# Kernel optimization log

Measured on AMD Instinct MI355X. Metric: run time of the kernel, lower is better.

The kernel has to match this reference:

```python
import jax, jax.numpy as jnp
import numpy as np


def setup_inputs() -> dict:
    key = jax.random.key(0)
    kq, kk, kv, km = jax.random.split(key, 4)
    B, H, S, D = 2, 16, 2048, 64
    q = jax.random.normal(kq, (B, H, S, D), dtype=jnp.float32)
    k = jax.random.normal(kk, (B, H, S, D), dtype=jnp.float32)
    v = jax.random.normal(kv, (B, H, S, D), dtype=jnp.float32)
    mask = jax.random.randint(km, (B, 1, S, S), 0, 2, dtype=jnp.int32)
    return {"q": q, "k": k, "v": v, "mask": mask}


def reference(q, k, v, mask):
    # Scaled dot-product attention: softmax(Q K^T / sqrt(D)) V
    D = q.shape[-1]
    scale = jnp.asarray(1.0 / np.sqrt(D), q.dtype)
    score = jnp.einsum("bhqd,bhkd->bhqk", q, k) * scale  # [B,H,S,S]
    score = jnp.where(mask == 0, jnp.asarray(-10000.0, score.dtype), score)
    attn = jax.nn.softmax(score, axis=-1)
    out = jnp.einsum("bhqk,bhkd->bhqd", attn, v)  # [B,H,S,D]
    return (out, attn)
```

## Files before the change

### kernel.cpp

```cpp
#include <hip/hip_runtime.h>
#include <stdint.h>

typedef __attribute__((ext_vector_type(8))) short short8;
typedef __attribute__((ext_vector_type(4))) float f32x4;

#define B_ 2
#define H_ 16
#define S_ 2048
#define D_ 64
#define KB_ 64
#define NT_ (S_ / KB_)

union PKU { unsigned u[4]; short8 s; };

__device__ __forceinline__ unsigned pk2(float x, float y) {
  const unsigned a = __builtin_bit_cast(unsigned, x) + 0x8000u;
  const unsigned b = __builtin_bit_cast(unsigned, y) + 0x8000u;
  return (a >> 16) | (b & 0xffff0000u);
}

__global__ __launch_bounds__(256, 4)
void attn_kernel(const float* __restrict__ Q, const float* __restrict__ K,
                 const float* __restrict__ V, const int* __restrict__ M,
                 float* __restrict__ O, float* __restrict__ A)
{
  const int bid = blockIdx.x + (blockIdx.y << 5);
  const int qt  = (bid >> 3) & 31;
  const int bh  = (bid & 7) | ((bid >> 8) << 3);
  const int b   = bh >> 4;

  const int tid  = threadIdx.x;
  const int wave = tid >> 6;
  const int lane = tid & 63;
  const int l15  = lane & 15;
  const int quad = lane >> 4;

  const float* Qp = Q + (size_t)bh * S_ * D_;
  const float* Kp = K + (size_t)bh * S_ * D_;
  const float* Vp = V + (size_t)bh * S_ * D_;
  const int*   Mp = M + (size_t)b * S_ * S_;
  float* Op = O + (size_t)bh * S_ * D_;
  float* Ap = A + (size_t)bh * S_ * S_;

  const int q0 = qt * 64 + wave * 16;

  __shared__ __attribute__((aligned(16))) short Ks[64][72];
  __shared__ __attribute__((aligned(16))) short Vt[64][72];
  __shared__ __attribute__((aligned(16))) float Ps[4][16][68];
  short* Pb = (short*)&Ps[wave][0][0];

  short8 aq[2];
  {
    const float* qr = Qp + (size_t)(q0 + l15) * D_ + quad * 8;
#pragma unroll
    for (int h = 0; h < 2; ++h) {
      const float4 x0 = *(const float4*)(qr + h * 32);
      const float4 x1 = *(const float4*)(qr + h * 32 + 4);
      PKU u;
      u.u[0] = pk2(x0.x * 0.125f, x0.y * 0.125f);
      u.u[1] = pk2(x0.z * 0.125f, x0.w * 0.125f);
      u.u[2] = pk2(x1.x * 0.125f, x1.y * 0.125f);
      u.u[3] = pk2(x1.z * 0.125f, x1.w * 0.125f);
      aq[h] = u.s;
    }
  }

  const int ksr  = tid >> 2;
  const int ksc  = (tid & 3) * 4;
  const int vd   = tid & 7;
  const int vk   = (tid >> 3) * 2;
  const int lrow = lane >> 4;
  const int lcol = (lane & 15) * 4;

  float kbuf[16];
  float vbuf[16];

  auto loadK = [&](int kt) {
#pragma unroll
    for (int j = 0; j < 4; ++j) {
      const float4 x = *(const float4*)(Kp + (size_t)(kt + ksr) * D_ + ksc + 16 * j);
      kbuf[4*j+0] = x.x; kbuf[4*j+1] = x.y; kbuf[4*j+2] = x.z; kbuf[4*j+3] = x.w;
    }
  };
  auto writeK = [&]() {
#pragma unroll
    for (int j = 0; j < 4; ++j)
      *(uint2*)&Ks[ksr][ksc + 16*j] =
        make_uint2(pk2(kbuf[4*j+0], kbuf[4*j+1]), pk2(kbuf[4*j+2], kbuf[4*j+3]));
  };
  auto loadV = [&](int kt) {
    const float* vr = Vp + (size_t)(kt + vk) * D_ + vd;
#pragma unroll
    for (int j = 0; j < 8; ++j) {
      vbuf[j]   = vr[8*j];
      vbuf[8+j] = vr[D_ + 8*j];
    }
  };
  auto writeV = [&]() {
#pragma unroll
    for (int j = 0; j < 8; ++j)
      *(unsigned*)&Vt[vd + 8*j][vk] = pk2(vbuf[j], vbuf[8+j]);
  };

  float lr[4];

  {
    float rowsum[4] = {0.f, 0.f, 0.f, 0.f};
    loadK(0);
    writeK();
    __syncthreads();
    for (int t = 0; t < NT_; ++t) {
      const int kt = t * KB_;
      if (t + 1 < NT_) loadK(kt + KB_);
      int4 mr[4];
#pragma unroll
      for (int i = 0; i < 4; ++i)
        mr[i] = *(const int4*)(Mp + (size_t)(q0 + lrow + 4*i) * S_ + kt + lcol);

      f32x4 acc[4] = {{0,0,0,0},{0,0,0,0},{0,0,0,0},{0,0,0,0}};
#pragma unroll
      for (int nt = 0; nt < 4; ++nt)
#pragma unroll
        for (int h = 0; h < 2; ++h) {
          const short8 bk = *(const short8*)&Ks[nt*16 + l15][h*32 + quad*8];
          acc[nt] = __builtin_amdgcn_mfma_f32_16x16x32_bf16(aq[h], bk, acc[nt], 0, 0, 0);
        }
#pragma unroll
      for (int nt = 0; nt < 4; ++nt)
#pragma unroll
        for (int r = 0; r < 4; ++r)
          Ps[wave][quad*4 + r][nt*16 + l15] = acc[nt][r];
      __asm__ volatile("s_waitcnt lgkmcnt(0)" ::: "memory");
#pragma unroll
      for (int i = 0; i < 4; ++i) {
        const f32x4 s = *(const f32x4*)&Ps[wave][lrow + 4*i][lcol];
        const float e0 = mr[i].x ? __expf(s[0]) : 0.f;
        const float e1 = mr[i].y ? __expf(s[1]) : 0.f;
        const float e2 = mr[i].z ? __expf(s[2]) : 0.f;
        const float e3 = mr[i].w ? __expf(s[3]) : 0.f;
        rowsum[i] += (e0 + e1) + (e2 + e3);
      }
      __syncthreads();
      if (t + 1 < NT_) writeK();
      __syncthreads();
    }
#pragma unroll
    for (int i = 0; i < 4; ++i) {
      float s = rowsum[i];
      s += __shfl_xor(s, 1);
      s += __shfl_xor(s, 2);
      s += __shfl_xor(s, 4);
      s += __shfl_xor(s, 8);
      lr[i] = (s > 0.f) ? -__logf(s) : 0.f;
    }
  }

  f32x4 oacc[4] = {{0,0,0,0},{0,0,0,0},{0,0,0,0},{0,0,0,0}};
  loadK(0);
  loadV(0);
  writeK();
  writeV();
  __syncthreads();
  for (int t = 0; t < NT_; ++t) {
    const int kt = t * KB_;
    if (t + 1 < NT_) { loadK(kt + KB_); loadV(kt + KB_); }
    int4 mr[4];
#pragma unroll
    for (int i = 0; i < 4; ++i)
      mr[i] = *(const int4*)(Mp + (size_t)(q0 + lrow + 4*i) * S_ + kt + lcol);

    f32x4 acc[4] = {{0,0,0,0},{0,0,0,0},{0,0,0,0},{0,0,0,0}};
#pragma unroll
    for (int nt = 0; nt < 4; ++nt)
#pragma unroll
      for (int h = 0; h < 2; ++h) {
        const short8 bk = *(const short8*)&Ks[nt*16 + l15][h*32 + quad*8];
        acc[nt] = __builtin_amdgcn_mfma_f32_16x16x32_bf16(aq[h], bk, acc[nt], 0, 0, 0);
      }
#pragma unroll
    for (int nt = 0; nt < 4; ++nt)
#pragma unroll
      for (int r = 0; r < 4; ++r)
        Ps[wave][quad*4 + r][nt*16 + l15] = acc[nt][r];
    __asm__ volatile("s_waitcnt lgkmcnt(0)" ::: "memory");

    f32x4 sr[4];
#pragma unroll
    for (int i = 0; i < 4; ++i)
      sr[i] = *(const f32x4*)&Ps[wave][lrow + 4*i][lcol];
    __asm__ volatile("s_waitcnt lgkmcnt(0)" ::: "memory");

#pragma unroll
    for (int i = 0; i < 4; ++i) {
      const float lv = lr[i];
      f32x4 p;
      p[0] = __expf(mr[i].x ? sr[i][0] + lv : -1e5f);
      p[1] = __expf(mr[i].y ? sr[i][1] + lv : -1e5f);
      p[2] = __expf(mr[i].z ? sr[i][2] + lv : -1e5f);
      p[3] = __expf(mr[i].w ? sr[i][3] + lv : -1e5f);
      __builtin_nontemporal_store(p, (f32x4*)(Ap + (size_t)(q0 + lrow + 4*i) * S_ + kt + lcol));
      *(uint2*)&Pb[(lrow + 4*i) * 72 + lcol] =
        make_uint2(pk2(p[0], p[1]), pk2(p[2], p[3]));
    }
    __asm__ volatile("s_waitcnt lgkmcnt(0)" ::: "memory");

    const short8 pa0 = *(const short8*)&Pb[l15 * 72 + quad * 8];
    const short8 pa1 = *(const short8*)&Pb[l15 * 72 + 32 + quad * 8];
#pragma unroll
    for (int nt = 0; nt < 4; ++nt) {
      const short8 bv0 = *(const short8*)&Vt[nt*16 + l15][quad*8];
      const short8 bv1 = *(const short8*)&Vt[nt*16 + l15][32 + quad*8];
      oacc[nt] = __builtin_amdgcn_mfma_f32_16x16x32_bf16(pa0, bv0, oacc[nt], 0, 0, 0);
      oacc[nt] = __builtin_amdgcn_mfma_f32_16x16x32_bf16(pa1, bv1, oacc[nt], 0, 0, 0);
    }
    __syncthreads();
    if (t + 1 < NT_) { writeK(); writeV(); }
    __syncthreads();
  }

#pragma unroll
  for (int nt = 0; nt < 4; ++nt)
#pragma unroll
    for (int r = 0; r < 4; ++r)
      Op[(size_t)(q0 + quad*4 + r) * D_ + nt*16 + l15] = oacc[nt][r];
}

extern "C" void kernel_launch(void* const* d_in, const int* in_sizes, int n_in,
                              void* d_out, int out_size, void* d_ws, size_t ws_size,
                              hipStream_t stream) {
  const float* q = (const float*)d_in[0];
  const float* k = (const float*)d_in[1];
  const float* v = (const float*)d_in[2];
  const int*   m = (const int*)d_in[3];
  float* out  = (float*)d_out;
  float* attn = out + (size_t)B_ * H_ * S_ * D_;

  dim3 grid(S_ / 64, B_ * H_);
  attn_kernel<<<grid, 256, 0, stream>>>(q, k, v, m, out, attn);
}
```

Baseline: 731.1 us.

## Vectorize V loads with swizzled transpose, add setprio, simplify P staging and barriers

V tiles are now loaded with coalesced float4 reads and transposed into LDS with an XOR swizzle on the key index, replacing strided scalar global loads. MFMA sections are wrapped in s_setprio to favour matrix issue. P is stored to LDS as fp32 and repacked to bf16 when read, instead of being written as bf16 into an aliased buffer. __syncthreads is replaced by a raw waitcnt+s_barrier. Scalar 16-bit LDS writes for V and the extra fp32 LDS traffic for P may add LDS cost.

```diff
diff --git a/kernel.cpp b/kernel.cpp
--- a/kernel.cpp
+++ b/kernel.cpp
@@ -11,12 +11,20 @@
 #define KB_ 64
 #define NT_ (S_ / KB_)
 
-union PKU { unsigned u[4]; short8 s; };
-
 __device__ __forceinline__ unsigned pk2(float x, float y) {
   const unsigned a = __builtin_bit_cast(unsigned, x) + 0x8000u;
   const unsigned b = __builtin_bit_cast(unsigned, y) + 0x8000u;
   return (a >> 16) | (b & 0xffff0000u);
+}
+__device__ __forceinline__ short b16(float x) {
+  return (short)((__builtin_bit_cast(unsigned, x) + 0x8000u) >> 16);
+}
+
+__device__ __forceinline__ void block_barrier() {
+  __asm__ volatile("s_waitcnt lgkmcnt(0)\n\ts_barrier" ::: "memory");
+}
+__device__ __forceinline__ void lgkm0() {
+  __asm__ volatile("s_waitcnt lgkmcnt(0)" ::: "memory");
 }
 
 __global__ __launch_bounds__(256, 4)
@@ -47,7 +55,6 @@
   __shared__ __attribute__((aligned(16))) short Ks[64][72];
   __shared__ __attribute__((aligned(16))) short Vt[64][72];
   __shared__ __attribute__((aligned(16))) float Ps[4][16][68];
-  short* Pb = (short*)&Ps[wave][0][0];
 
   short8 aq[2];
   {
@@ -56,7 +63,7 @@
     for (int h = 0; h < 2; ++h) {
       const float4 x0 = *(const float4*)(qr + h * 32);
       const float4 x1 = *(const float4*)(qr + h * 32 + 4);
-      PKU u;
+      union { unsigned u[4]; short8 s; } u;
       u.u[0] = pk2(x0.x * 0.125f, x0.y * 0.125f);
       u.u[1] = pk2(x0.z * 0.125f, x0.w * 0.125f);
       u.u[2] = pk2(x1.x * 0.125f, x1.y * 0.125f);
@@ -65,10 +72,8 @@
     }
   }
 
-  const int ksr  = tid >> 2;
-  const int ksc  = (tid & 3) * 4;
-  const int vd   = tid & 7;
-  const int vk   = (tid >> 3) * 2;
+  const int srow = tid >> 2;
+  const int scol = (tid & 3) * 4;
   const int lrow = lane >> 4;
   const int lcol = (lane & 15) * 4;
 
@@ -78,28 +83,31 @@
   auto loadK = [&](int kt) {
 #pragma unroll
     for (int j = 0; j < 4; ++j) {
-      const float4 x = *(const float4*)(Kp + (size_t)(kt + ksr) * D_ + ksc + 16 * j);
+      const float4 x = *(const float4*)(Kp + (size_t)(kt + srow) * D_ + scol + 16 * j);
       kbuf[4*j+0] = x.x; kbuf[4*j+1] = x.y; kbuf[4*j+2] = x.z; kbuf[4*j+3] = x.w;
     }
   };
   auto writeK = [&]() {
 #pragma unroll
     for (int j = 0; j < 4; ++j)
-      *(uint2*)&Ks[ksr][ksc + 16*j] =
+      *(uint2*)&Ks[srow][scol + 16*j] =
         make_uint2(pk2(kbuf[4*j+0], kbuf[4*j+1]), pk2(kbuf[4*j+2], kbuf[4*j+3]));
   };
   auto loadV = [&](int kt) {
-    const float* vr = Vp + (size_t)(kt + vk) * D_ + vd;
-#pragma unroll
-    for (int j = 0; j < 8; ++j) {
-      vbuf[j]   = vr[8*j];
-      vbuf[8+j] = vr[D_ + 8*j];
+#pragma unroll
+    for (int u = 0; u < 4; ++u) {
+      const float4 x = *(const float4*)(Vp + (size_t)(kt + srow) * D_ + scol + 16 * u);
+      vbuf[4*u+0] = x.x; vbuf[4*u+1] = x.y; vbuf[4*u+2] = x.z; vbuf[4*u+3] = x.w;
     }
   };
   auto writeV = [&]() {
 #pragma unroll
-    for (int j = 0; j < 8; ++j)
-      *(unsigned*)&Vt[vd + 8*j][vk] = pk2(vbuf[j], vbuf[8+j]);
+    for (int u = 0; u < 4; ++u) {
+      const int kks = srow ^ (u << 4);
+#pragma unroll
+      for (int c = 0; c < 4; ++c)
+        Vt[16*u + scol + c][kks] = b16(vbuf[4*u+c]);
+    }
   };
 
   float lr[4];
@@ -108,7 +116,7 @@
     float rowsum[4] = {0.f, 0.f, 0.f, 0.f};
     loadK(0);
     writeK();
-    __syncthreads();
+    block_barrier();
     for (int t = 0; t < NT_; ++t) {
       const int kt = t * KB_;
       if (t + 1 < NT_) loadK(kt + KB_);
@@ -118,6 +126,7 @@
         mr[i] = *(const int4*)(Mp + (size_t)(q0 + lrow + 4*i) * S_ + kt + lcol);
 
       f32x4 acc[4] = {{0,0,0,0},{0,0,0,0},{0,0,0,0},{0,0,0,0}};
+      __builtin_amdgcn_s_setprio(1);
 #pragma unroll
       for (int nt = 0; nt < 4; ++nt)
 #pragma unroll
@@ -125,12 +134,13 @@
           const short8 bk = *(const short8*)&Ks[nt*16 + l15][h*32 + quad*8];
           acc[nt] = __builtin_amdgcn_mfma_f32_16x16x32_bf16(aq[h], bk, acc[nt], 0, 0, 0);
         }
+      __builtin_amdgcn_s_setprio(0);
 #pragma unroll
       for (int nt = 0; nt < 4; ++nt)
 #pragma unroll
         for (int r = 0; r < 4; ++r)
           Ps[wave][quad*4 + r][nt*16 + l15] = acc[nt][r];
-      __asm__ volatile("s_waitcnt lgkmcnt(0)" ::: "memory");
+      lgkm0();
 #pragma unroll
       for (int i = 0; i < 4; ++i) {
         const f32x4 s = *(const f32x4*)&Ps[wave][lrow + 4*i][lcol];
@@ -140,9 +150,9 @@
         const float e3 = mr[i].w ? __expf(s[3]) : 0.f;
         rowsum[i] += (e0 + e1) + (e2 + e3);
       }
-      __syncthreads();
+      block_barrier();
       if (t + 1 < NT_) writeK();
-      __syncthreads();
+      block_barrier();
     }
 #pragma unroll
     for (int i = 0; i < 4; ++i) {
@@ -160,7 +170,7 @@
   loadV(0);
   writeK();
   writeV();
-  __syncthreads();
+  block_barrier();
   for (int t = 0; t < NT_; ++t) {
     const int kt = t * KB_;
     if (t + 1 < NT_) { loadK(kt + KB_); loadV(kt + KB_); }
@@ -170,6 +180,7 @@
       mr[i] = *(const int4*)(Mp + (size_t)(q0 + lrow + 4*i) * S_ + kt + lcol);
 
     f32x4 acc[4] = {{0,0,0,0},{0,0,0,0},{0,0,0,0},{0,0,0,0}};
+    __builtin_amdgcn_s_setprio(1);
 #pragma unroll
     for (int nt = 0; nt < 4; ++nt)
 #pragma unroll
@@ -177,45 +188,53 @@
         const short8 bk = *(const short8*)&Ks[nt*16 + l15][h*32 + quad*8];
         acc[nt] = __builtin_amdgcn_mfma_f32_16x16x32_bf16(aq[h], bk, acc[nt], 0, 0, 0);
       }
+    __builtin_amdgcn_s_setprio(0);
 #pragma unroll
     for (int nt = 0; nt < 4; ++nt)
 #pragma unroll
       for (int r = 0; r < 4; ++r)
         Ps[wave][quad*4 + r][nt*16 + l15] = acc[nt][r];
-    __asm__ volatile("s_waitcnt lgkmcnt(0)" ::: "memory");
-
-    f32x4 sr[4];
-#pragma unroll
-    for (int i = 0; i < 4; ++i)
-      sr[i] = *(const f32x4*)&Ps[wave][lrow + 4*i][lcol];
-    __asm__ volatile("s_waitcnt lgkmcnt(0)" ::: "memory");
+    lgkm0();
 
 #pragma unroll
     for (int i = 0; i < 4; ++i) {
+      const f32x4 s = *(const f32x4*)&Ps[wave][lrow + 4*i][lcol];
       const float lv = lr[i];
       f32x4 p;
-      p[0] = __expf(mr[i].x ? sr[i][0] + lv : -1e5f);
-      p[1] = __expf(mr[i].y ? sr[i][1] + lv : -1e5f);
-      p[2] = __expf(mr[i].z ? sr[i][2] + lv : -1e5f);
-      p[3] = __expf(mr[i].w ? sr[i][3] + lv : -1e5f);
+      p[0] = __expf(mr[i].x ? s[0] + lv : -1e5f);
+      p[1] = __expf(mr[i].y ? s[1] + lv : -1e5f);
+      p[2] = __expf(mr[i].z ? s[2] + lv : -1e5f);
+      p[3] = __expf(mr[i].w ? s[3] + lv : -1e5f);
       __builtin_nontemporal_store(p, (f32x4*)(Ap + (size_t)(q0 + lrow + 4*i) * S_ + kt + lcol));
-      *(uint2*)&Pb[(lrow + 4*i) * 72 + lcol] =
-        make_uint2(pk2(p[0], p[1]), pk2(p[2], p[3]));
-    }
-    __asm__ volatile("s_waitcnt lgkmcnt(0)" ::: "memory");
-
-    const short8 pa0 = *(const short8*)&Pb[l15 * 72 + quad * 8];
-    const short8 pa1 = *(const short8*)&Pb[l15 * 72 + 32 + quad * 8];
+      *(f32x4*)&Ps[wave][lrow + 4*i][lcol] = p;
+    }
+    lgkm0();
+
+    short8 pa0, pa1;
+    {
+      const f32x4 q0v = *(const f32x4*)&Ps[wave][l15][quad*8];
+      const f32x4 q1v = *(const f32x4*)&Ps[wave][l15][quad*8 + 4];
+      const f32x4 q2v = *(const f32x4*)&Ps[wave][l15][32 + quad*8];
+      const f32x4 q3v = *(const f32x4*)&Ps[wave][l15][32 + quad*8 + 4];
+      union { unsigned u[4]; short8 s; } ua, ub;
+      ua.u[0] = pk2(q0v[0], q0v[1]); ua.u[1] = pk2(q0v[2], q0v[3]);
+      ua.u[2] = pk2(q1v[0], q1v[1]); ua.u[3] = pk2(q1v[2], q1v[3]);
+      ub.u[0] = pk2(q2v[0], q2v[1]); ub.u[1] = pk2(q2v[2], q2v[3]);
+      ub.u[2] = pk2(q3v[0], q3v[1]); ub.u[3] = pk2(q3v[2], q3v[3]);
+      pa0 = ua.s; pa1 = ub.s;
+    }
+    __builtin_amdgcn_s_setprio(1);
 #pragma unroll
     for (int nt = 0; nt < 4; ++nt) {
-      const short8 bv0 = *(const short8*)&Vt[nt*16 + l15][quad*8];
-      const short8 bv1 = *(const short8*)&Vt[nt*16 + l15][32 + quad*8];
+      const short8 bv0 = *(const short8*)&Vt[nt*16 + l15][(quad*8) ^ (nt << 4)];
+      const short8 bv1 = *(const short8*)&Vt[nt*16 + l15][(32 + quad*8) ^ (nt << 4)];
       oacc[nt] = __builtin_amdgcn_mfma_f32_16x16x32_bf16(pa0, bv0, oacc[nt], 0, 0, 0);
       oacc[nt] = __builtin_amdgcn_mfma_f32_16x16x32_bf16(pa1, bv1, oacc[nt], 0, 0, 0);
     }
-    __syncthreads();
+    __builtin_amdgcn_s_setprio(0);
+    block_barrier();
     if (t + 1 < NT_) { writeK(); writeV(); }
-    __syncthreads();
+    block_barrier();
   }
 
 #pragma unroll
```

Measured after the change: 736.9 us. About the same (+0.8%).
